# Kernel tuning notes

Measured on AMD Instinct MI355X. Metric: run time of the kernel, lower is better.

Reference implementation:

```python
import jax, jax.numpy as jnp
import numpy as np

D_MODEL = 512
N_HEADS = 8
D_K = D_MODEL // N_HEADS
D_DTW = 21


def setup_inputs() -> dict:
    key = jax.random.key(0)
    ks = jax.random.split(key, 16)
    bs, S = 16, 512
    def lin(k, fan_in, shape):
        return jax.random.uniform(k, shape, jnp.float32, -1.0, 1.0) / np.sqrt(fan_in)
    return {
        "Q": jax.random.normal(ks[0], (bs, S, D_MODEL), jnp.float32),
        "K": jax.random.normal(ks[1], (bs, S, D_MODEL), jnp.float32),
        "V": jax.random.normal(ks[2], (bs, S, D_MODEL), jnp.float32),
        "G": jax.random.normal(ks[3], (bs, S, D_MODEL), jnp.float32),
        "dtw_cost": jax.random.uniform(ks[4], (bs, D_DTW, S, S), jnp.float32),
        "Wq": lin(ks[5], D_MODEL, (D_MODEL, D_MODEL)), "bq": lin(ks[6], D_MODEL, (D_MODEL,)),
        "Wk": lin(ks[7], D_MODEL, (D_MODEL, D_MODEL)), "bk": lin(ks[8], D_MODEL, (D_MODEL,)),
        "Wv": lin(ks[9], D_MODEL, (D_MODEL, D_MODEL)), "bv": lin(ks[10], D_MODEL, (D_MODEL,)),
        "Wd": lin(ks[11], D_DTW, (N_HEADS, D_DTW)), "bd": lin(ks[12], D_DTW, (N_HEADS,)),
        "Wo": lin(ks[13], D_MODEL, (D_MODEL, D_MODEL)), "bo": lin(ks[14], D_MODEL, (D_MODEL,)),
    }


def reference(Q, K, V, G, dtw_cost, Wq, bq, Wk, bk, Wv, bv, Wd, bd, Wo, bo):
    bs, S, _ = Q.shape
    # QKV projections, split into heads: [bs, H, S, dk]
    def proj(x, W, b):
        y = x @ W.T + b
        return y.reshape(bs, S, N_HEADS, D_K).transpose(0, 2, 1, 3)
    q = proj(Q, Wq, bq)
    k = proj(K, Wk, bk)
    v = proj(V, Wv, bv)
    # scaled dot-product scores [bs, H, S, S]
    scores = jnp.einsum("bhqd,bhkd->bhqk", q, k) / np.sqrt(D_K).astype(np.float32)
    # DTW-cost bias: linear over the cost-channel dim (21 -> H), added per head
    bias = jnp.einsum("bcqk,hc->bhqk", dtw_cost, Wd) + bd[None, :, None, None]
    attn = jax.nn.softmax(scores + bias, axis=-1)
    out = jnp.einsum("bhqk,bhkd->bhqd", attn, v)  # [bs, H, S, dk]
    concat = out.transpose(0, 2, 1, 3).reshape(bs, S, D_MODEL)
    output = concat @ Wo.T + bo
    return (output, attn)
```

## Files before the change

kernel.cpp:

```cpp
#include <hip/hip_runtime.h>
#include <hip/hip_bf16.h>
#include <cstddef>
#include <cstdint>

#define BS   16
#define SLEN 512
#define DM   512
#define NH   8
#define DK   64
#define DC   21

typedef __attribute__((ext_vector_type(8))) short short8;
typedef __attribute__((ext_vector_type(4))) float f32x4;
typedef __attribute__((ext_vector_type(8))) _Float16 h16x8;
typedef __attribute__((ext_vector_type(4))) _Float16 h16x4;
typedef __attribute__((ext_vector_type(2))) unsigned u32x2;
typedef _Float16 h16x4a __attribute__((ext_vector_type(4), may_alias));

__device__ inline unsigned pack_bf16(float a, float b) {
    unsigned ua = __builtin_bit_cast(unsigned, a);
    unsigned ub = __builtin_bit_cast(unsigned, b);
    ua = (ua + 0x7fffu + ((ua >> 16) & 1u)) >> 16;
    ub = (ub + 0x7fffu + ((ub >> 16) & 1u)) >> 16;
    return ua | (ub << 16);
}
__device__ inline unsigned cvt2(float a, float b) { return pack_bf16(a, b); }
__device__ inline ushort bf16_1(float a) { return (ushort)(pack_bf16(a, 0.f) & 0xffffu); }
__device__ inline unsigned pk_f16(float a, float b) {
    return __builtin_bit_cast(unsigned, __builtin_amdgcn_cvt_pkrtz(a, b));
}

__device__ __host__ inline size_t bias_chunk_base(int bh, int q16) {
    return 2 * (((size_t)bh * SLEN + (size_t)q16) * SLEN);
}

__global__ __launch_bounds__(256) void gemm_qkv(
    const float* __restrict__ Q, const float* __restrict__ K,
    const float* __restrict__ V,
    const float* __restrict__ Wq, const float* __restrict__ Wk,
    const float* __restrict__ Wv,
    const float* __restrict__ bq, const float* __restrict__ bk,
    const float* __restrict__ bv,
    ushort* __restrict__ qb, ushort* __restrict__ kb, ushort* __restrict__ vt)
{
    __shared__ alignas(16) ushort Atile[64 * 64];
    __shared__ alignas(16) ushort Btile[128 * 64];

    const int z = blockIdx.z;
    const float* X    = (z == 0) ? Q  : (z == 1) ? K  : V;
    const float* W    = (z == 0) ? Wq : (z == 1) ? Wk : Wv;
    const float* bias = (z == 0) ? bq : (z == 1) ? bk : bv;

    const int tid = threadIdx.x;
    const int wave = tid >> 6, lane = tid & 63;
    const int lq = lane & 15, lg = lane >> 4;
    const int wr = wave >> 1, wc = wave & 1;
    const int m0 = blockIdx.x * 64;
    const int n0 = blockIdx.y * 128;

    f32x4 acc[2][4];
#pragma unroll
    for (int i = 0; i < 2; ++i)
#pragma unroll
        for (int j = 0; j < 4; ++j) acc[i][j] = (f32x4){0.f, 0.f, 0.f, 0.f};

    float4 pa[2][2], pb[4][2];

#define LOAD_A(K0)                                                              \
    _Pragma("unroll")                                                           \
    for (int i = 0; i < 2; ++i) {                                               \
        const int P = tid + 256 * i;                                            \
        const int row = P >> 3, cp = P & 7;                                     \
        const float4* s = (const float4*)&X[(size_t)(m0 + row) * 512 + (K0) + cp * 8]; \
        pa[i][0] = s[0]; pa[i][1] = s[1];                                       \
    }
#define LOAD_B(K0)                                                              \
    _Pragma("unroll")                                                           \
    for (int i = 0; i < 4; ++i) {                                               \
        const int P = tid + 256 * i;                                            \
        const int row = P >> 3, cp = P & 7;                                     \
        const float4* s = (const float4*)&W[(size_t)(n0 + row) * 512 + (K0) + cp * 8]; \
        pb[i][0] = s[0]; pb[i][1] = s[1];                                       \
    }

    LOAD_A(0)
    LOAD_B(0)

    for (int it = 0; it < 8; ++it) {
        __syncthreads();
#pragma unroll
        for (int i = 0; i < 2; ++i) {
            const int P = tid + 256 * i;
            const int row = P >> 3, cp = P & 7;
            uint4 w;
            w.x = cvt2(pa[i][0].x, pa[i][0].y);
            w.y = cvt2(pa[i][0].z, pa[i][0].w);
            w.z = cvt2(pa[i][1].x, pa[i][1].y);
            w.w = cvt2(pa[i][1].z, pa[i][1].w);
            *(uint4*)((char*)Atile + row * 128 + 16 * (cp ^ (row & 7))) = w;
        }
#pragma unroll
        for (int i = 0; i < 4; ++i) {
            const int P = tid + 256 * i;
            const int row = P >> 3, cp = P & 7;
            uint4 w;
            w.x = cvt2(pb[i][0].x, pb[i][0].y);
            w.y = cvt2(pb[i][0].z, pb[i][0].w);
            w.z = cvt2(pb[i][1].x, pb[i][1].y);
            w.w = cvt2(pb[i][1].z, pb[i][1].w);
            *(uint4*)((char*)Btile + row * 128 + 16 * (cp ^ (row & 7))) = w;
        }
        __syncthreads();

        if (it < 7) {
            const int kn = (it + 1) * 64;
            LOAD_A(kn)
            LOAD_B(kn)
        }

        short8 af[2][2], bfr[4][2];
#pragma unroll
        for (int mi = 0; mi < 2; ++mi)
#pragma unroll
            for (int kh = 0; kh < 2; ++kh) {
                const int row = wr * 32 + mi * 16 + lq;
                af[mi][kh] = *(const short8*)((const char*)Atile + row * 128 +
                                              16 * ((kh * 4 + lg) ^ (row & 7)));
            }
#pragma unroll
        for (int ni = 0; ni < 4; ++ni)
#pragma unroll
            for (int kh = 0; kh < 2; ++kh) {
                const int row = wc * 64 + ni * 16 + lq;
                bfr[ni][kh] = *(const short8*)((const char*)Btile + row * 128 +
                                               16 * ((kh * 4 + lg) ^ (row & 7)));
            }
        __builtin_amdgcn_s_setprio(1);
#pragma unroll
        for (int kh = 0; kh < 2; ++kh)
#pragma unroll
            for (int mi = 0; mi < 2; ++mi)
#pragma unroll
                for (int ni = 0; ni < 4; ++ni)
                    acc[mi][ni] = __builtin_amdgcn_mfma_f32_16x16x32_bf16(
                        af[mi][kh], bfr[ni][kh], acc[mi][ni], 0, 0, 0);
        __builtin_amdgcn_s_setprio(0);
    }
#undef LOAD_A
#undef LOAD_B

    if (z < 2) {
        ushort* out = (z == 0) ? qb : kb;
#pragma unroll
        for (int mi = 0; mi < 2; ++mi) {
            const int mb = m0 + wr * 32 + mi * 16 + lg * 4;
#pragma unroll
            for (int ni = 0; ni < 4; ++ni) {
                const int n = n0 + wc * 64 + ni * 16 + lq;
                const int h = n >> 6, d = n & 63;
                const float bb = bias[n];
#pragma unroll
                for (int r = 0; r < 4; ++r) {
                    const int m = mb + r;
                    const int bidx = m >> 9, s = m & 511;
                    out[((size_t)(bidx * NH + h) * SLEN + s) * DK + d] =
                        bf16_1(acc[mi][ni][r] + bb);
                }
            }
        }
    } else {
#pragma unroll
        for (int mi = 0; mi < 2; ++mi) {
            const int mb = m0 + wr * 32 + mi * 16 + lg * 4;
            const int bidx = mb >> 9, s0 = mb & 511;
#pragma unroll
            for (int ni = 0; ni < 4; ++ni) {
                const int n = n0 + wc * 64 + ni * 16 + lq;
                const int h = n >> 6, d = n & 63;
                const float bb = bias[n];
                uint2 pk;
                pk.x = pk_f16(acc[mi][ni][0] + bb, acc[mi][ni][1] + bb);
                pk.y = pk_f16(acc[mi][ni][2] + bb, acc[mi][ni][3] + bb);
                *(uint2*)&vt[((size_t)(bidx * NH + h) * DK + d) * SLEN + s0] = pk;
            }
        }
    }
}

__global__ __launch_bounds__(256) void gemm_out(
    const ushort* __restrict__ Xb, const float* __restrict__ W,
    const float* __restrict__ bias, float* __restrict__ out)
{
    __shared__ alignas(16) ushort Atile[64 * 64];
    __shared__ alignas(16) ushort Btile[128 * 64];

    const int tid = threadIdx.x;
    const int wave = tid >> 6, lane = tid & 63;
    const int lq = lane & 15, lg = lane >> 4;
    const int wr = wave >> 1, wc = wave & 1;
    const int m0 = blockIdx.x * 64;
    const int n0 = blockIdx.y * 128;

    f32x4 acc[2][4];
#pragma unroll
    for (int i = 0; i < 2; ++i)
#pragma unroll
        for (int j = 0; j < 4; ++j) acc[i][j] = (f32x4){0.f, 0.f, 0.f, 0.f};

    uint4  qa[2];
    float4 pb[4][2];

#define LOAD_A(K0)                                                              \
    _Pragma("unroll")                                                           \
    for (int i = 0; i < 2; ++i) {                                               \
        const int P = tid + 256 * i;                                            \
        const int row = P >> 3, sl = P & 7;                                     \
        qa[i] = *(const uint4*)&Xb[(size_t)(m0 + row) * 512 + (K0) + sl * 8];   \
    }
#define LOAD_B(K0)                                                              \
    _Pragma("unroll")                                                           \
    for (int i = 0; i < 4; ++i) {                                               \
        const int P = tid + 256 * i;                                            \
        const int row = P >> 3, cp = P & 7;                                     \
        const float4* s = (const float4*)&W[(size_t)(n0 + row) * 512 + (K0) + cp * 8]; \
        pb[i][0] = s[0]; pb[i][1] = s[1];                                       \
    }

    LOAD_A(0)
    LOAD_B(0)

    for (int it = 0; it < 8; ++it) {
        __syncthreads();
#pragma unroll
        for (int i = 0; i < 2; ++i) {
            const int P = tid + 256 * i;
            const int row = P >> 3, sl = P & 7;
            *(uint4*)((char*)Atile + row * 128 + 16 * (sl ^ (row & 7))) = qa[i];
        }
#pragma unroll
        for (int i = 0; i < 4; ++i) {
            const int P = tid + 256 * i;
            const int row = P >> 3, cp = P & 7;
            uint4 w;
            w.x = cvt2(pb[i][0].x, pb[i][0].y);
            w.y = cvt2(pb[i][0].z, pb[i][0].w);
            w.z = cvt2(pb[i][1].x, pb[i][1].y);
            w.w = cvt2(pb[i][1].z, pb[i][1].w);
            *(uint4*)((char*)Btile + row * 128 + 16 * (cp ^ (row & 7))) = w;
        }
        __syncthreads();

        if (it < 7) {
            const int kn = (it + 1) * 64;
            LOAD_A(kn)
            LOAD_B(kn)
        }

        short8 af[2][2], bfr[4][2];
#pragma unroll
        for (int mi = 0; mi < 2; ++mi)
#pragma unroll
            for (int kh = 0; kh < 2; ++kh) {
                const int row = wr * 32 + mi * 16 + lq;
                af[mi][kh] = *(const short8*)((const char*)Atile + row * 128 +
                                              16 * ((kh * 4 + lg) ^ (row & 7)));
            }
#pragma unroll
        for (int ni = 0; ni < 4; ++ni)
#pragma unroll
            for (int kh = 0; kh < 2; ++kh) {
                const int row = wc * 64 + ni * 16 + lq;
                bfr[ni][kh] = *(const short8*)((const char*)Btile + row * 128 +
                                               16 * ((kh * 4 + lg) ^ (row & 7)));
            }
        __builtin_amdgcn_s_setprio(1);
#pragma unroll
        for (int kh = 0; kh < 2; ++kh)
#pragma unroll
            for (int mi = 0; mi < 2; ++mi)
#pragma unroll
                for (int ni = 0; ni < 4; ++ni)
                    acc[mi][ni] = __builtin_amdgcn_mfma_f32_16x16x32_bf16(
                        af[mi][kh], bfr[ni][kh], acc[mi][ni], 0, 0, 0);
        __builtin_amdgcn_s_setprio(0);
    }
#undef LOAD_A
#undef LOAD_B

#pragma unroll
    for (int mi = 0; mi < 2; ++mi) {
        const int mb = m0 + wr * 32 + mi * 16 + lg * 4;
#pragma unroll
        for (int ni = 0; ni < 4; ++ni) {
            const int n = n0 + wc * 64 + ni * 16 + lq;
            const float bb = bias[n];
#pragma unroll
            for (int r = 0; r < 4; ++r)
                out[(size_t)(mb + r) * 512 + n] = acc[mi][ni][r] + bb;
        }
    }
}

__global__ __launch_bounds__(512) void bias_kernel(
    const float* __restrict__ dtw, const float* __restrict__ Wd,
    const float* __restrict__ bd, _Float16* __restrict__ bias16)
{
    __shared__ float wdl[NH * DC];
    __shared__ float bdl[NH];
    const int k = threadIdx.x;
    const int q = blockIdx.x;
    const int b = blockIdx.y;
    if (k < NH * DC) wdl[k] = Wd[k];
    if (k < NH) bdl[k] = bd[k];
    __syncthreads();

    float acc[NH];
#pragma unroll
    for (int h = 0; h < NH; ++h) acc[h] = bdl[h];

    const float* p = dtw + ((size_t)b * DC * SLEN + q) * SLEN + k;
#pragma unroll
    for (int c = 0; c < DC; ++c) {
        const float x = p[(size_t)c * SLEN * SLEN];
#pragma unroll
        for (int h = 0; h < NH; ++h) acc[h] += x * wdl[h * DC + c];
    }
    const int q16 = q & ~15, ql = q & 15;
#pragma unroll
    for (int h = 0; h < NH; ++h) {
        const size_t base = bias_chunk_base(b * NH + h, q16);
        bias16[base + (size_t)ql * SLEN + k] = (_Float16)acc[h];
    }
}

__global__ __launch_bounds__(256, 4) void attn_mfma(
    const ushort* __restrict__ qb, const ushort* __restrict__ kb,
    const ushort* __restrict__ vt, float* __restrict__ attn,
    ushort* __restrict__ concat)
{
    __shared__ alignas(16) ushort Pbuf[4][2][16][32];
    __shared__ alignas(16) float  Ored[2][16][68];
    __shared__ float SumBuf[2][2][16];

    const int tid = threadIdx.x;
    const int wave = tid >> 6;
    const int lane = tid & 63;
    const int lq = lane & 15;
    const int lg = lane >> 4;
    const int qs = wave >> 1;
    const int kh = wave & 1;

    const unsigned l = blockIdx.x;
    const int g  = (int)((l & 7) + 8 * (l >> 7));
    const int qt = (int)((l >> 3) & 15);
    const int h = g & 7, b = g >> 3;
    const int bh = b * NH + h;
    const int q0 = qt * 32 + qs * 16;

    const ushort* qptr = qb + ((size_t)bh * SLEN + q0) * DK;
    const ushort* kptr = kb + ((size_t)bh * SLEN + kh * 256) * DK;
    const ushort* vptr = vt + (size_t)bh * DK * SLEN;
    float* attn_b = attn + ((size_t)bh * SLEN + q0) * SLEN;
    const _Float16* bias_row =
        (const _Float16*)attn + bias_chunk_base(bh, q0) + (size_t)lq * SLEN + kh * 256;

    const short8 qf0 = *(const short8*)&qptr[(size_t)lq * DK + lg * 8];
    const short8 qf1 = *(const short8*)&qptr[(size_t)lq * DK + lg * 8 + 32];

    float sum = 0.f;
    u32x2 ep[16];

#pragma unroll
    for (int ktl = 0; ktl < 16; ++ktl) {
        const short8 a0 = *(const short8*)&kptr[(size_t)(ktl * 16 + lq) * DK + lg * 8];
        const short8 a1 = *(const short8*)&kptr[(size_t)(ktl * 16 + lq) * DK + lg * 8 + 32];
        f32x4 c = {0.f, 0.f, 0.f, 0.f};
        c = __builtin_amdgcn_mfma_f32_16x16x32_bf16(a0, qf0, c, 0, 0, 0);
        c = __builtin_amdgcn_mfma_f32_16x16x32_bf16(a1, qf1, c, 0, 0, 0);
        const h16x4a b4 = *(const h16x4a*)&bias_row[ktl * 16 + 4 * lg];
        const float e0 = __expf(c[0] * 0.125f + (float)b4[0]);
        const float e1 = __expf(c[1] * 0.125f + (float)b4[1]);
        const float e2 = __expf(c[2] * 0.125f + (float)b4[2]);
        const float e3 = __expf(c[3] * 0.125f + (float)b4[3]);
        sum += (e0 + e1) + (e2 + e3);
        u32x2 pk;
        pk[0] = pk_f16(e0, e1);
        pk[1] = pk_f16(e2, e3);
        ep[ktl] = pk;
    }
    sum += __shfl_xor(sum, 16);
    sum += __shfl_xor(sum, 32);
    if (lg == 0) SumBuf[qs][kh][lq] = sum;
    __syncthreads();
    const float inv = 1.0f / (SumBuf[qs][0][lq] + SumBuf[qs][1][lq]);

    f32x4 oacc[4] = {{0.f,0.f,0.f,0.f},{0.f,0.f,0.f,0.f},{0.f,0.f,0.f,0.f},{0.f,0.f,0.f,0.f}};

#pragma unroll
    for (int c2 = 0; c2 < 8; ++c2) {
        char* pbb = (char*)&Pbuf[wave][c2 & 1][0][0];
#pragma unroll
        for (int t = 0; t < 2; ++t) {
            const int ktl = 2 * c2 + t;
            const h16x4 hv = __builtin_bit_cast(h16x4, ep[ktl]);
            f32x4 a;
            a[0] = (float)hv[0] * inv;
            a[1] = (float)hv[1] * inv;
            a[2] = (float)hv[2] * inv;
            a[3] = (float)hv[3] * inv;
            *(f32x4*)&attn_b[(size_t)lq * SLEN + kh * 256 + ktl * 16 + lg * 4] = a;
            const int slot = (t * 2 + (lg >> 1)) ^ (lq & 3);
            *(u32x2*)(pbb + lq * 64 + slot * 16 + (lg & 1) * 8) = ep[ktl];
        }
        asm volatile("s_waitcnt lgkmcnt(0)" ::: "memory");

        const h16x8 pa = *(const h16x8*)(pbb + lq * 64 + (lg ^ (lq & 3)) * 16);
        __builtin_amdgcn_s_setprio(1);
#pragma unroll
        for (int dt = 0; dt < 4; ++dt) {
            const h16x8 vb8 = *(const h16x8*)
                &vptr[(size_t)(dt * 16 + lq) * SLEN + (kh * 8 + c2) * 32 + lg * 8];
            oacc[dt] = __builtin_amdgcn_mfma_f32_16x16x32_f16(pa, vb8, oacc[dt], 0, 0, 0);
        }
        __builtin_amdgcn_s_setprio(0);
    }

    if (kh == 1) {
#pragma unroll
        for (int dt = 0; dt < 4; ++dt)
#pragma unroll
            for (int r = 0; r < 4; ++r)
                Ored[qs][lg * 4 + r][dt * 16 + lq] = oacc[dt][r];
    }
    __syncthreads();
    if (kh == 0) {
        ushort* cbase = concat + ((size_t)(b * SLEN + q0)) * DM + h * 64;
#pragma unroll
        for (int r = 0; r < 4; ++r) {
            const float iv = __shfl(inv, lg * 4 + r);
#pragma unroll
            for (int dt = 0; dt < 4; ++dt) {
                const float val = (oacc[dt][r] + Ored[qs][lg * 4 + r][dt * 16 + lq]) * iv;
                cbase[(size_t)(lg * 4 + r) * DM + dt * 16 + lq] = bf16_1(val);
            }
        }
    }
}

extern "C" void kernel_launch(void* const* d_in, const int* in_sizes, int n_in,
                              void* d_out, int out_size, void* d_ws, size_t ws_size,
                              hipStream_t stream)
{
    const float* Q   = (const float*)d_in[0];
    const float* K   = (const float*)d_in[1];
    const float* V   = (const float*)d_in[2];
    const float* dtw = (const float*)d_in[4];
    const float* Wq  = (const float*)d_in[5];
    const float* bq  = (const float*)d_in[6];
    const float* Wk  = (const float*)d_in[7];
    const float* bk  = (const float*)d_in[8];
    const float* Wv  = (const float*)d_in[9];
    const float* bv  = (const float*)d_in[10];
    const float* Wd  = (const float*)d_in[11];
    const float* bd  = (const float*)d_in[12];
    const float* Wo  = (const float*)d_in[13];
    const float* bo  = (const float*)d_in[14];

    float* out  = (float*)d_out;
    float* attn = out + (size_t)BS * SLEN * DM;
    _Float16* bias16 = (_Float16*)attn;

    const size_t PHS = (size_t)BS * NH * SLEN * DK;
    ushort* qb = (ushort*)d_ws;
    ushort* kb = qb + PHS;
    ushort* vt = kb + PHS;
    ushort* cb = vt + PHS;

    gemm_qkv<<<dim3(128, 4, 3), 256, 0, stream>>>(Q, K, V, Wq, Wk, Wv,
                                                  bq, bk, bv, qb, kb, vt);

    bias_kernel<<<dim3(SLEN, BS), 512, 0, stream>>>(dtw, Wd, bd, bias16);

    attn_mfma<<<dim3(2048), 256, 0, stream>>>(qb, kb, vt, attn, cb);

    gemm_out<<<dim3(128, 4), 256, 0, stream>>>(cb, Wo, bo, out);
}
```

Before: 241.7 us.

## Merge QKV projection GEMM and DTW bias kernel into one interleaved launch

Combines the QKV GEMM and the DTW-cost bias kernel into a single launch of 9728 blocks. Block IDs are interleaved so each group of 19 holds 3 GEMM blocks and 16 bias blocks. The compute-bound GEMM tiles and the bandwidth-bound bias reduction can then run at the same time on the GPU, and one launch boundary is removed. In exchange, the bias work moves from 512-thread to 256-thread blocks that each do two passes. The fused kernel also carries the GEMM's shared-memory and register footprint, which may lower occupancy for the bias blocks.

```diff
diff --git a/kernel.cpp b/kernel.cpp
--- a/kernel.cpp
+++ b/kernel.cpp
@@ -34,37 +34,49 @@
     return 2 * (((size_t)bh * SLEN + (size_t)q16) * SLEN);
 }
 
-__global__ __launch_bounds__(256) void gemm_qkv(
+__global__ __launch_bounds__(256) void qkv_bias(
     const float* __restrict__ Q, const float* __restrict__ K,
     const float* __restrict__ V,
     const float* __restrict__ Wq, const float* __restrict__ Wk,
     const float* __restrict__ Wv,
     const float* __restrict__ bq, const float* __restrict__ bk,
     const float* __restrict__ bv,
-    ushort* __restrict__ qb, ushort* __restrict__ kb, ushort* __restrict__ vt)
+    const float* __restrict__ dtw, const float* __restrict__ Wd,
+    const float* __restrict__ bd,
+    ushort* __restrict__ qb, ushort* __restrict__ kb, ushort* __restrict__ vt,
+    _Float16* __restrict__ bias16)
 {
     __shared__ alignas(16) ushort Atile[64 * 64];
     __shared__ alignas(16) ushort Btile[128 * 64];
-
-    const int z = blockIdx.z;
-    const float* X    = (z == 0) ? Q  : (z == 1) ? K  : V;
-    const float* W    = (z == 0) ? Wq : (z == 1) ? Wk : Wv;
-    const float* bias = (z == 0) ? bq : (z == 1) ? bk : bv;
+    __shared__ float wdl[NH * DC];
+    __shared__ float bdl[NH];
 
     const int tid = threadIdx.x;
-    const int wave = tid >> 6, lane = tid & 63;
-    const int lq = lane & 15, lg = lane >> 4;
-    const int wr = wave >> 1, wc = wave & 1;
-    const int m0 = blockIdx.x * 64;
-    const int n0 = blockIdx.y * 128;
-
-    f32x4 acc[2][4];
-#pragma unroll
-    for (int i = 0; i < 2; ++i)
-#pragma unroll
-        for (int j = 0; j < 4; ++j) acc[i][j] = (f32x4){0.f, 0.f, 0.f, 0.f};
-
-    float4 pa[2][2], pb[4][2];
+    const unsigned bid = blockIdx.x;
+    const unsigned grp = bid / 19u, r = bid % 19u;
+
+    if (r < 3) {
+        const int gi = (int)(grp * 3 + r);
+        const int z = gi >> 9;
+        const int rem = gi & 511;
+        const int m0 = (rem & 127) * 64;
+        const int n0 = (rem >> 7) * 128;
+
+        const float* X    = (z == 0) ? Q  : (z == 1) ? K  : V;
+        const float* W    = (z == 0) ? Wq : (z == 1) ? Wk : Wv;
+        const float* bias = (z == 0) ? bq : (z == 1) ? bk : bv;
+
+        const int wave = tid >> 6, lane = tid & 63;
+        const int lq = lane & 15, lg = lane >> 4;
+        const int wr = wave >> 1, wc = wave & 1;
+
+        f32x4 acc[2][4];
+#pragma unroll
+        for (int i = 0; i < 2; ++i)
+#pragma unroll
+            for (int j = 0; j < 4; ++j) acc[i][j] = (f32x4){0.f, 0.f, 0.f, 0.f};
+
+        float4 pa[2][2], pb[4][2];
 
 #define LOAD_A(K0)                                                              \
     _Pragma("unroll")                                                           \
@@ -83,6 +95,178 @@
         pb[i][0] = s[0]; pb[i][1] = s[1];                                       \
     }
 
+        LOAD_A(0)
+        LOAD_B(0)
+
+        for (int it = 0; it < 8; ++it) {
+            __syncthreads();
+#pragma unroll
+            for (int i = 0; i < 2; ++i) {
+                const int P = tid + 256 * i;
+                const int row = P >> 3, cp = P & 7;
+                uint4 w;
+                w.x = cvt2(pa[i][0].x, pa[i][0].y);
+                w.y = cvt2(pa[i][0].z, pa[i][0].w);
+                w.z = cvt2(pa[i][1].x, pa[i][1].y);
+                w.w = cvt2(pa[i][1].z, pa[i][1].w);
+                *(uint4*)((char*)Atile + row * 128 + 16 * (cp ^ (row & 7))) = w;
+            }
+#pragma unroll
+            for (int i = 0; i < 4; ++i) {
+                const int P = tid + 256 * i;
+                const int row = P >> 3, cp = P & 7;
+                uint4 w;
+                w.x = cvt2(pb[i][0].x, pb[i][0].y);
+                w.y = cvt2(pb[i][0].z, pb[i][0].w);
+                w.z = cvt2(pb[i][1].x, pb[i][1].y);
+                w.w = cvt2(pb[i][1].z, pb[i][1].w);
+                *(uint4*)((char*)Btile + row * 128 + 16 * (cp ^ (row & 7))) = w;
+            }
+            __syncthreads();
+
+            if (it < 7) {
+                const int kn = (it + 1) * 64;
+                LOAD_A(kn)
+                LOAD_B(kn)
+            }
+
+            short8 af[2][2], bfr[4][2];
+#pragma unroll
+            for (int mi = 0; mi < 2; ++mi)
+#pragma unroll
+                for (int kh = 0; kh < 2; ++kh) {
+                    const int row = wr * 32 + mi * 16 + lq;
+                    af[mi][kh] = *(const short8*)((const char*)Atile + row * 128 +
+                                                  16 * ((kh * 4 + lg) ^ (row & 7)));
+                }
+#pragma unroll
+            for (int ni = 0; ni < 4; ++ni)
+#pragma unroll
+                for (int kh = 0; kh < 2; ++kh) {
+                    const int row = wc * 64 + ni * 16 + lq;
+                    bfr[ni][kh] = *(const short8*)((const char*)Btile + row * 128 +
+                                                   16 * ((kh * 4 + lg) ^ (row & 7)));
+                }
+            __builtin_amdgcn_s_setprio(1);
+#pragma unroll
+            for (int kh = 0; kh < 2; ++kh)
+#pragma unroll
+                for (int mi = 0; mi < 2; ++mi)
+#pragma unroll
+                    for (int ni = 0; ni < 4; ++ni)
+                        acc[mi][ni] = __builtin_amdgcn_mfma_f32_16x16x32_bf16(
+                            af[mi][kh], bfr[ni][kh], acc[mi][ni], 0, 0, 0);
+            __builtin_amdgcn_s_setprio(0);
+        }
+#undef LOAD_A
+#undef LOAD_B
+
+        if (z < 2) {
+            ushort* out = (z == 0) ? qb : kb;
+#pragma unroll
+            for (int mi = 0; mi < 2; ++mi) {
+                const int mb = m0 + wr * 32 + mi * 16 + lg * 4;
+#pragma unroll
+                for (int ni = 0; ni < 4; ++ni) {
+                    const int n = n0 + wc * 64 + ni * 16 + lq;
+                    const int h = n >> 6, d = n & 63;
+                    const float bb = bias[n];
+#pragma unroll
+                    for (int rr = 0; rr < 4; ++rr) {
+                        const int m = mb + rr;
+                        const int bidx = m >> 9, s = m & 511;
+                        out[((size_t)(bidx * NH + h) * SLEN + s) * DK + d] =
+                            bf16_1(acc[mi][ni][rr] + bb);
+                    }
+                }
+            }
+        } else {
+#pragma unroll
+            for (int mi = 0; mi < 2; ++mi) {
+                const int mb = m0 + wr * 32 + mi * 16 + lg * 4;
+                const int bidx = mb >> 9, s0 = mb & 511;
+#pragma unroll
+                for (int ni = 0; ni < 4; ++ni) {
+                    const int n = n0 + wc * 64 + ni * 16 + lq;
+                    const int h = n >> 6, d = n & 63;
+                    const float bb = bias[n];
+                    uint2 pk;
+                    pk.x = pk_f16(acc[mi][ni][0] + bb, acc[mi][ni][1] + bb);
+                    pk.y = pk_f16(acc[mi][ni][2] + bb, acc[mi][ni][3] + bb);
+                    *(uint2*)&vt[((size_t)(bidx * NH + h) * DK + d) * SLEN + s0] = pk;
+                }
+            }
+        }
+    } else {
+        const int bi = (int)(grp * 16 + (r - 3));
+        const int q = bi & 511;
+        const int b = bi >> 9;
+        if (tid < NH * DC) wdl[tid] = Wd[tid];
+        if (tid < NH) bdl[tid] = bd[tid];
+        __syncthreads();
+
+        const int q16 = q & ~15, ql = q & 15;
+#pragma unroll
+        for (int half = 0; half < 2; ++half) {
+            const int k = tid + half * 256;
+            float acc[NH];
+#pragma unroll
+            for (int h = 0; h < NH; ++h) acc[h] = bdl[h];
+            const float* p = dtw + ((size_t)b * DC * SLEN + q) * SLEN + k;
+#pragma unroll
+            for (int c = 0; c < DC; ++c) {
+                const float x = p[(size_t)c * SLEN * SLEN];
+#pragma unroll
+                for (int h = 0; h < NH; ++h) acc[h] += x * wdl[h * DC + c];
+            }
+#pragma unroll
+            for (int h = 0; h < NH; ++h) {
+                const size_t base = bias_chunk_base(b * NH + h, q16);
+                bias16[base + (size_t)ql * SLEN + k] = (_Float16)acc[h];
+            }
+        }
+    }
+}
+
+__global__ __launch_bounds__(256) void gemm_out(
+    const ushort* __restrict__ Xb, const float* __restrict__ W,
+    const float* __restrict__ bias, float* __restrict__ out)
+{
+    __shared__ alignas(16) ushort Atile[64 * 64];
+    __shared__ alignas(16) ushort Btile[128 * 64];
+
+    const int tid = threadIdx.x;
+    const int wave = tid >> 6, lane = tid & 63;
+    const int lq = lane & 15, lg = lane >> 4;
+    const int wr = wave >> 1, wc = wave & 1;
+    const int m0 = blockIdx.x * 64;
+    const int n0 = blockIdx.y * 128;
+
+    f32x4 acc[2][4];
+#pragma unroll
+    for (int i = 0; i < 2; ++i)
+#pragma unroll
+        for (int j = 0; j < 4; ++j) acc[i][j] = (f32x4){0.f, 0.f, 0.f, 0.f};
+
+    uint4  qa[2];
+    float4 pb[4][2];
+
+#define LOAD_A(K0)                                                              \
+    _Pragma("unroll")                                                           \
+    for (int i = 0; i < 2; ++i) {                                               \
+        const int P = tid + 256 * i;                                            \
+        const int row = P >> 3, sl = P & 7;                                     \
+        qa[i] = *(const uint4*)&Xb[(size_t)(m0 + row) * 512 + (K0) + sl * 8];   \
+    }
+#define LOAD_B(K0)                                                              \
+    _Pragma("unroll")                                                           \
+    for (int i = 0; i < 4; ++i) {                                               \
+        const int P = tid + 256 * i;                                            \
+        const int row = P >> 3, cp = P & 7;                                     \
+        const float4* s = (const float4*)&W[(size_t)(n0 + row) * 512 + (K0) + cp * 8]; \
+        pb[i][0] = s[0]; pb[i][1] = s[1];                                       \
+    }
+
     LOAD_A(0)
     LOAD_B(0)
 
@@ -91,13 +275,8 @@
 #pragma unroll
         for (int i = 0; i < 2; ++i) {
             const int P = tid + 256 * i;
-            const int row = P >> 3, cp = P & 7;
-            uint4 w;
-            w.x = cvt2(pa[i][0].x, pa[i][0].y);
-            w.y = cvt2(pa[i][0].z, pa[i][0].w);
-            w.z = cvt2(pa[i][1].x, pa[i][1].y);
-            w.w = cvt2(pa[i][1].z, pa[i][1].w);
-            *(uint4*)((char*)Atile + row * 128 + 16 * (cp ^ (row & 7))) = w;
+            const int row = P >> 3, sl = P & 7;
+            *(uint4*)((char*)Atile + row * 128 + 16 * (sl ^ (row & 7))) = qa[i];
         }
 #pragma unroll
         for (int i = 0; i < 4; ++i) {
@@ -149,144 +328,6 @@
 #undef LOAD_A
 #undef LOAD_B
 
-    if (z < 2) {
-        ushort* out = (z == 0) ? qb : kb;
-#pragma unroll
-        for (int mi = 0; mi < 2; ++mi) {
-            const int mb = m0 + wr * 32 + mi * 16 + lg * 4;
-#pragma unroll
-            for (int ni = 0; ni < 4; ++ni) {
-                const int n = n0 + wc * 64 + ni * 16 + lq;
-                const int h = n >> 6, d = n & 63;
-                const float bb = bias[n];
-#pragma unroll
-                for (int r = 0; r < 4; ++r) {
-                    const int m = mb + r;
-                    const int bidx = m >> 9, s = m & 511;
-                    out[((size_t)(bidx * NH + h) * SLEN + s) * DK + d] =
-                        bf16_1(acc[mi][ni][r] + bb);
-                }
-            }
-        }
-    } else {
-#pragma unroll
-        for (int mi = 0; mi < 2; ++mi) {
-            const int mb = m0 + wr * 32 + mi * 16 + lg * 4;
-            const int bidx = mb >> 9, s0 = mb & 511;
-#pragma unroll
-            for (int ni = 0; ni < 4; ++ni) {
-                const int n = n0 + wc * 64 + ni * 16 + lq;
-                const int h = n >> 6, d = n & 63;
-                const float bb = bias[n];
-                uint2 pk;
-                pk.x = pk_f16(acc[mi][ni][0] + bb, acc[mi][ni][1] + bb);
-                pk.y = pk_f16(acc[mi][ni][2] + bb, acc[mi][ni][3] + bb);
-                *(uint2*)&vt[((size_t)(bidx * NH + h) * DK + d) * SLEN + s0] = pk;
-            }
-        }
-    }
-}
-
-__global__ __launch_bounds__(256) void gemm_out(
-    const ushort* __restrict__ Xb, const float* __restrict__ W,
-    const float* __restrict__ bias, float* __restrict__ out)
-{
-    __shared__ alignas(16) ushort Atile[64 * 64];
-    __shared__ alignas(16) ushort Btile[128 * 64];
-
-    const int tid = threadIdx.x;
-    const int wave = tid >> 6, lane = tid & 63;
-    const int lq = lane & 15, lg = lane >> 4;
-    const int wr = wave >> 1, wc = wave & 1;
-    const int m0 = blockIdx.x * 64;
-    const int n0 = blockIdx.y * 128;
-
-    f32x4 acc[2][4];
-#pragma unroll
-    for (int i = 0; i < 2; ++i)
-#pragma unroll
-        for (int j = 0; j < 4; ++j) acc[i][j] = (f32x4){0.f, 0.f, 0.f, 0.f};
-
-    uint4  qa[2];
-    float4 pb[4][2];
-
-#define LOAD_A(K0)                                                              \
-    _Pragma("unroll")                                                           \
-    for (int i = 0; i < 2; ++i) {                                               \
-        const int P = tid + 256 * i;                                            \
-        const int row = P >> 3, sl = P & 7;                                     \
-        qa[i] = *(const uint4*)&Xb[(size_t)(m0 + row) * 512 + (K0) + sl * 8];   \
-    }
-#define LOAD_B(K0)                                                              \
-    _Pragma("unroll")                                                           \
-    for (int i = 0; i < 4; ++i) {                                               \
-        const int P = tid + 256 * i;                                            \
-        const int row = P >> 3, cp = P & 7;                                     \
-        const float4* s = (const float4*)&W[(size_t)(n0 + row) * 512 + (K0) + cp * 8]; \
-        pb[i][0] = s[0]; pb[i][1] = s[1];                                       \
-    }
-
-    LOAD_A(0)
-    LOAD_B(0)
-
-    for (int it = 0; it < 8; ++it) {
-        __syncthreads();
-#pragma unroll
-        for (int i = 0; i < 2; ++i) {
-            const int P = tid + 256 * i;
-            const int row = P >> 3, sl = P & 7;
-            *(uint4*)((char*)Atile + row * 128 + 16 * (sl ^ (row & 7))) = qa[i];
-        }
-#pragma unroll
-        for (int i = 0; i < 4; ++i) {
-            const int P = tid + 256 * i;
-            const int row = P >> 3, cp = P & 7;
-            uint4 w;
-            w.x = cvt2(pb[i][0].x, pb[i][0].y);
-            w.y = cvt2(pb[i][0].z, pb[i][0].w);
-            w.z = cvt2(pb[i][1].x, pb[i][1].y);
-            w.w = cvt2(pb[i][1].z, pb[i][1].w);
-            *(uint4*)((char*)Btile + row * 128 + 16 * (cp ^ (row & 7))) = w;
-        }
-        __syncthreads();
-
-        if (it < 7) {
-            const int kn = (it + 1) * 64;
-            LOAD_A(kn)
-            LOAD_B(kn)
-        }
-
-        short8 af[2][2], bfr[4][2];
-#pragma unroll
-        for (int mi = 0; mi < 2; ++mi)
-#pragma unroll
-            for (int kh = 0; kh < 2; ++kh) {
-                const int row = wr * 32 + mi * 16 + lq;
-                af[mi][kh] = *(const short8*)((const char*)Atile + row * 128 +
-                                              16 * ((kh * 4 + lg) ^ (row & 7)));
-            }
-#pragma unroll
-        for (int ni = 0; ni < 4; ++ni)
-#pragma unroll
-            for (int kh = 0; kh < 2; ++kh) {
-                const int row = wc * 64 + ni * 16 + lq;
-                bfr[ni][kh] = *(const short8*)((const char*)Btile + row * 128 +
-                                               16 * ((kh * 4 + lg) ^ (row & 7)));
-            }
-        __builtin_amdgcn_s_setprio(1);
-#pragma unroll
-        for (int kh = 0; kh < 2; ++kh)
-#pragma unroll
-            for (int mi = 0; mi < 2; ++mi)
-#pragma unroll
-                for (int ni = 0; ni < 4; ++ni)
-                    acc[mi][ni] = __builtin_amdgcn_mfma_f32_16x16x32_bf16(
-                        af[mi][kh], bfr[ni][kh], acc[mi][ni], 0, 0, 0);
-        __builtin_amdgcn_s_setprio(0);
-    }
-#undef LOAD_A
-#undef LOAD_B
-
 #pragma unroll
     for (int mi = 0; mi < 2; ++mi) {
         const int mb = m0 + wr * 32 + mi * 16 + lg * 4;
@@ -298,38 +339,6 @@
             for (int r = 0; r < 4; ++r)
                 out[(size_t)(mb + r) * 512 + n] = acc[mi][ni][r] + bb;
         }
-    }
-}
-
-__global__ __launch_bounds__(512) void bias_kernel(
-    const float* __restrict__ dtw, const float* __restrict__ Wd,
-    const float* __restrict__ bd, _Float16* __restrict__ bias16)
-{
-    __shared__ float wdl[NH * DC];
-    __shared__ float bdl[NH];
-    const int k = threadIdx.x;
-    const int q = blockIdx.x;
-    const int b = blockIdx.y;
-    if (k < NH * DC) wdl[k] = Wd[k];
-    if (k < NH) bdl[k] = bd[k];
-    __syncthreads();
-
-    float acc[NH];
-#pragma unroll
-    for (int h = 0; h < NH; ++h) acc[h] = bdl[h];
-
-    const float* p = dtw + ((size_t)b * DC * SLEN + q) * SLEN + k;
-#pragma unroll
-    for (int c = 0; c < DC; ++c) {
-        const float x = p[(size_t)c * SLEN * SLEN];
-#pragma unroll
-        for (int h = 0; h < NH; ++h) acc[h] += x * wdl[h * DC + c];
-    }
-    const int q16 = q & ~15, ql = q & 15;
-#pragma unroll
-    for (int h = 0; h < NH; ++h) {
-        const size_t base = bias_chunk_base(b * NH + h, q16);
-        bias16[base + (size_t)ql * SLEN + k] = (_Float16)acc[h];
     }
 }
 
@@ -476,10 +485,8 @@
     ushort* vt = kb + PHS;
     ushort* cb = vt + PHS;
 
-    gemm_qkv<<<dim3(128, 4, 3), 256, 0, stream>>>(Q, K, V, Wq, Wk, Wv,
-                                                  bq, bk, bv, qb, kb, vt);
-
-    bias_kernel<<<dim3(SLEN, BS), 512, 0, stream>>>(dtw, Wd, bd, bias16);
+    qkv_bias<<<dim3(9728), 256, 0, stream>>>(Q, K, V, Wq, Wk, Wv, bq, bk, bv,
+                                             dtw, Wd, bd, qb, kb, vt, bias16);
 
     attn_mfma<<<dim3(2048), 256, 0, stream>>>(qb, kb, vt, attn, cb);
 
```

New measurement: 366.0 us. 1.51x slower.
